# Optimization experiments

Hardware: AMD Instinct MI355X
Metric: run time of the kernel (lower is better)

Reference implementation:

```python
import jax, jax.numpy as jnp
import numpy as np

K = 7          # kernel_size
PAD = K // 2
NAZ, NEL = 12, 5
HID = 64
IC = 2         # input_channels == num_instruments
OC = 2         # output_channels (stereo)
EPS = 1e-5


def conv1d_same(x, w, b):
    # x: (N, Cin, T), w: (Cout, Cin, K) -> (N, Cout, T); cross-correlation like torch
    y = jax.lax.conv_general_dilated(x, w, (1,), 'SAME',
                                     dimension_numbers=('NCH', 'OIH', 'NCH'))
    return y + b[None, :, None]


def batchnorm(x, g, bt):
    # training-mode BatchNorm1d: biased batch stats over (N, T)
    mean = x.mean(axis=(0, 2), keepdims=True)
    var = x.var(axis=(0, 2), keepdims=True)
    return (x - mean) * jax.lax.rsqrt(var + EPS) * g[None, :, None] + bt[None, :, None]


def lrelu(x):
    return jnp.where(x >= 0, x, 0.2 * x)


def setup_inputs() -> dict:
    key = jax.random.key(0)
    ks = jax.random.split(key, 16)
    d = {}
    d['x'] = jax.random.normal(ks[0], (8, IC, 131072), dtype=jnp.float32)
    # spatial_param_net
    d['W1'] = jax.random.normal(ks[1], (HID, IC, K), dtype=jnp.float32) * 0.1
    d['b1'] = jnp.zeros((HID,), jnp.float32)
    d['g1'] = jnp.ones((HID,), jnp.float32)
    d['be1'] = jnp.zeros((HID,), jnp.float32)
    d['W2'] = jax.random.normal(ks[2], (2 * HID, HID, K), dtype=jnp.float32) * 0.05
    d['b2'] = jnp.zeros((2 * HID,), jnp.float32)
    d['g2'] = jnp.ones((2 * HID,), jnp.float32)
    d['be2'] = jnp.zeros((2 * HID,), jnp.float32)
    d['W3'] = jax.random.normal(ks[3], (IC * 3, 2 * HID, K), dtype=jnp.float32) * 0.05
    d['b3'] = jnp.zeros((IC * 3,), jnp.float32)
    # HRTF table: (num_azimuth*num_elevation, output_channels, K)
    d['hrtf'] = jax.random.normal(ks[4], (NAZ * NEL, OC, K), dtype=jnp.float32)
    # binaural_renderer (first conv in-channels = input_channels = 2)
    d['RW1'] = jax.random.normal(ks[5], (HID, IC, K), dtype=jnp.float32) * 0.1
    d['rb1'] = jnp.zeros((HID,), jnp.float32)
    d['rg1'] = jnp.ones((HID,), jnp.float32)
    d['rbe1'] = jnp.zeros((HID,), jnp.float32)
    d['RW2'] = jax.random.normal(ks[6], (2 * HID, HID, K), dtype=jnp.float32) * 0.05
    d['rb2'] = jnp.zeros((2 * HID,), jnp.float32)
    d['rg2'] = jnp.ones((2 * HID,), jnp.float32)
    d['rbe2'] = jnp.zeros((2 * HID,), jnp.float32)
    d['RW3'] = jax.random.normal(ks[7], (OC, 2 * HID, K), dtype=jnp.float32) * 0.05
    d['rb3'] = jnp.zeros((OC,), jnp.float32)
    return d


def reference(x, W1, b1, g1, be1, W2, b2, g2, be2, W3, b3, hrtf,
              RW1, rb1, rg1, rbe1, RW2, rb2, rg2, rbe2, RW3, rb3):
    B, I, T = x.shape
    # spatial parameter network
    h = lrelu(batchnorm(conv1d_same(x, W1, b1), g1, be1))
    h = lrelu(batchnorm(conv1d_same(h, W2, b2), g2, be2))
    sp = jnp.tanh(conv1d_same(h, W3, b3)).reshape(B, I, 3, T)
    # only t=0 of azimuth/elevation/distance is used (matches torch loop)
    az = (sp[:, :, 0, 0] + 1.0) * 0.5 * (NAZ - 1)
    el = (sp[:, :, 1, 0] + 1.0) * 0.5 * (NEL - 1)
    dist = (sp[:, :, 2, 0] + 1.0) * 0.5 * 0.9 + 0.1      # (B, I)
    az_i = jnp.clip(az.astype(jnp.int32), 0, NAZ - 1)
    el_i = jnp.clip(el.astype(jnp.int32), 0, NEL - 1)
    idx = el_i * NAZ + az_i                               # (B, I)
    wg = hrtf[idx]                                        # (B, I, OC, K) gathered filters
    # per-(b,i) conv1d with its gathered HRTF filter, scale by distance, sum over instruments
    xp = jnp.pad(x, ((0, 0), (0, 0), (PAD, PAD)))
    windows = jnp.stack([xp[:, :, k:k + T] for k in range(K)], axis=2)  # (B, I, K, T)
    summed = jnp.einsum('bikt,bick,bi->bct', windows, wg, dist)          # (B, OC, T)
    # binaural renderer
    h = lrelu(batchnorm(conv1d_same(summed, RW1, rb1), rg1, rbe1))
    h = lrelu(batchnorm(conv1d_same(h, RW2, rb2), rg2, rbe2))
    return jnp.tanh(conv1d_same(h, RW3, rb3))
```

## Files before the change

### kernel.cpp

```cpp
#include <hip/hip_runtime.h>
#include <hip/hip_fp16.h>
#include <cstddef>


#define TLEN 131072
#define NB 8
#define NICH 2
#define NHID 64
#define NH2 128
#define EPSV 1e-5f
#define CNTF 1048576.0f
#define FT 120
#define FGRID 1093
#define XCH 1024
#define NCH 128
#define XGRID 1024

typedef _Float16 f16x8 __attribute__((ext_vector_type(8)));
typedef float f32x4 __attribute__((ext_vector_type(4)));

__device__ __forceinline__ float lrelu(float v) { return fmaxf(v, 0.2f * v); }
__device__ __forceinline__ unsigned short h16(float v) {
  return __half_as_ushort(__float2half(v));
}
__device__ __forceinline__ float fh16(unsigned short u) {
  return __half2float(__ushort_as_half(u));
}
__device__ __forceinline__ float ftanh(float x) {
  float e = __expf(2.f * x);
  return 1.f - 2.f / (e + 1.f);
}

__global__ __launch_bounds__(256) void prep_weights(
    const float* __restrict__ W2c, const float* __restrict__ RW2c,
    const float* __restrict__ RW3c,
    const float* __restrict__ W1c, const float* __restrict__ RW1c,
    unsigned short* __restrict__ w2sp, unsigned short* __restrict__ w2re,
    unsigned short* __restrict__ w3g,
    unsigned short* __restrict__ w1sp, unsigned short* __restrict__ w1re)
{
  int e = blockIdx.x * 256 + threadIdx.x;
  if (e < 114688) {
    int e2 = (e >= 57344) ? e - 57344 : e;
    int frag = e2 >> 9, within = e2 & 511;
    int c = frag >> 3, mt = frag & 7;
    int mn = within >> 5, kk = within & 31;
    int o = mt * 16 + mn;
    int tap = c >> 1, ch = (c & 1) * 32 + kk;
    const float* src = (e >= 57344) ? RW2c : W2c;
    unsigned short* dst = (e >= 57344) ? w2re : w2sp;
    dst[e2] = h16(src[(o * 64 + ch) * 7 + tap]);
  } else if (e < 116736) {
    int e2 = e - 114688;
    int c = e2 >> 9, within = e2 & 511;
    int m = within >> 5, kk = within & 31;
    int ch = c * 32 + kk;
    w3g[e2] = (m < 14) ? h16(RW3c[((m / 7) * 128 + ch) * 7 + (m % 7)])
                       : (unsigned short)0;
  } else if (e < 120832) {
    int e2 = e - 116736;
    int which = (e2 >= 2048);
    int e3 = e2 & 2047;
    int m = e3 >> 9, w = e3 & 511;
    int mn = w >> 5, K = w & 31;
    int i = K >> 4, kk = K & 15;
    const float* src = which ? RW1c : W1c;
    unsigned short* dst = which ? w1re : w1sp;
    dst[e3] = (kk < 7) ? h16(src[(m * 16 + mn) * 14 + i * 7 + kk])
                       : (unsigned short)0;
  }
}

__global__ __launch_bounds__(256) void xcorr_stats(
    const float* __restrict__ z, float* __restrict__ partials)
{
  const int b = blockIdx.x >> 7;
  const int t0 = (blockIdx.x & (NCH - 1)) * XCH;
  __shared__ float zs[2][XCH + 8];
  __shared__ float redx[4][30];
  #pragma unroll
  for (int i = 0; i < 2; ++i) {
    const float* zp = &z[(size_t)(b * 2 + i) * TLEN + t0];
    *(float4*)&zs[i][threadIdx.x * 4] =
        *(const float4*)&zp[threadIdx.x * 4];
    if (threadIdx.x < 7) {
      int tg = t0 + XCH + threadIdx.x;
      zs[i][XCH + threadIdx.x] =
          (tg < TLEN) ? z[(size_t)(b * 2 + i) * TLEN + tg] : 0.f;
    }
    if (threadIdx.x == 7) zs[i][XCH + 7] = 0.f;
  }
  __syncthreads();

  float acc[30];
  #pragma unroll
  for (int q = 0; q < 30; ++q) acc[q] = 0.f;
  const int tb = threadIdx.x * 4;
  #pragma unroll
  for (int tt = 0; tt < 4; ++tt) {
    int j = tb + tt;
    float z0 = zs[0][j], z1 = zs[1][j];
    acc[28] += z0; acc[29] += z1;
    #pragma unroll
    for (int d = 0; d < 7; ++d) {
      float a0 = zs[0][j + d], a1 = zs[1][j + d];
      acc[d]      += z0 * a0;
      acc[7 + d]  += z0 * a1;
      acc[14 + d] += z1 * a0;
      acc[21 + d] += z1 * a1;
    }
  }
  #pragma unroll
  for (int q = 0; q < 30; ++q)
    #pragma unroll
    for (int m = 1; m <= 32; m <<= 1)
      acc[q] += __shfl_xor(acc[q], m, 64);
  const int lane = threadIdx.x & 63, wv = threadIdx.x >> 6;
  if (lane == 0)
    #pragma unroll
    for (int q = 0; q < 30; ++q) redx[wv][q] = acc[q];
  __syncthreads();
  if (threadIdx.x < 30)
    partials[blockIdx.x * 30 + threadIdx.x] =
        redx[0][threadIdx.x] + redx[1][threadIdx.x] +
        redx[2][threadIdx.x] + redx[3][threadIdx.x];
}

__global__ __launch_bounds__(256) void assemble_coef1(
    const float* __restrict__ partials, int nblocks,
    const float* __restrict__ W1c, const float* __restrict__ b1c,
    const float* __restrict__ g, const float* __restrict__ be,
    float* __restrict__ coef)
{
  __shared__ float R[30];
  __shared__ float pr[8][30];
  __shared__ float w1s[64 * 14];
  for (int e = threadIdx.x; e < 64 * 14; e += 256) w1s[e] = W1c[e];
  if (threadIdx.x < 240) {
    int q = threadIdx.x % 30, chunk = threadIdx.x / 30;
    float s = 0.f;
    for (int j = chunk; j < nblocks; j += 8) s += partials[j * 30 + q];
    pr[chunk][q] = s;
  }
  __syncthreads();
  if (threadIdx.x < 30) {
    float s = 0.f;
    #pragma unroll
    for (int c = 0; c < 8; ++c) s += pr[c][threadIdx.x];
    R[threadIdx.x] = s;
  }
  __syncthreads();
  if (threadIdx.x < 64) {
    int o = threadIdx.x;
    const float* w = &w1s[o * 14];
    float b1v = b1c[o];
    float sy = 0.f;
    #pragma unroll
    for (int i = 0; i < 2; ++i)
      #pragma unroll
      for (int k = 0; k < 7; ++k) sy += w[i * 7 + k] * R[28 + i];
    float syy = 0.f;
    #pragma unroll
    for (int i = 0; i < 2; ++i)
      #pragma unroll
      for (int k = 0; k < 7; ++k) {
        float wv = w[i * 7 + k];
        #pragma unroll
        for (int i2 = 0; i2 < 2; ++i2)
          #pragma unroll
          for (int k2 = 0; k2 < 7; ++k2) {
            int d = k2 - k;
            float r = (d >= 0) ? R[i * 14 + i2 * 7 + d]
                               : R[i2 * 14 + i * 7 - d];
            syy += wv * w[i2 * 7 + k2] * r;
          }
      }
    float S1 = CNTF * b1v + sy;
    float S2 = 2.f * b1v * S1 - CNTF * b1v * b1v + syy;
    float mean = S1 / CNTF;
    float var = S2 / CNTF - mean * mean;
    float a = g[o] * rsqrtf(var + EPSV);
    coef[o] = a;
    coef[64 + o] = be[o] - mean * a;
  }
}

__global__ __launch_bounds__(256) void reduce_coef(
    const float* __restrict__ partials, int nblocks, int C,
    const float* __restrict__ bso,
    const float* __restrict__ g, const float* __restrict__ be,
    float* __restrict__ coef)
{
  const int c = blockIdx.x;
  float s = 0.f, ss = 0.f;
  for (int j = threadIdx.x; j < nblocks; j += 256) {
    s  += partials[j * 2 * C + c];
    ss += partials[j * 2 * C + C + c];
  }
  #pragma unroll
  for (int off = 32; off >= 1; off >>= 1) {
    s  += __shfl_down(s, off, 64);
    ss += __shfl_down(ss, off, 64);
  }
  __shared__ float rs[4], rss[4];
  const int lane = threadIdx.x & 63, wv = threadIdx.x >> 6;
  if (lane == 0) { rs[wv] = s; rss[wv] = ss; }
  __syncthreads();
  if (threadIdx.x == 0) {
    float st  = rs[0] + rs[1] + rs[2] + rs[3];
    float sst = rss[0] + rss[1] + rss[2] + rss[3];
    float mean = st / CNTF;
    float var  = sst / CNTF - mean * mean;
    float a = g[c] * rsqrtf(var + EPSV);
    float d = be[c] - mean * a;
    coef[c] = a;
    coef[C + c] = d;
    coef[2 * C + c] = d + a * bso[c];
  }
}

__device__ __forceinline__ void stage_x(
    int t0, int xoff, const float* __restrict__ xin, int b, float* xs)
{
  for (int e = threadIdx.x; e < 2 * 168; e += 256) {
    int i = e / 168, j = e % 168;
    int tg = t0 - xoff + j;
    xs[e] = (tg >= 0 && tg < TLEN) ? xin[(b * NICH + i) * TLEN + tg] : 0.f;
  }
}

template<int HOF>
__device__ __forceinline__ void h1_mfma(
    int t0, const float* xs, unsigned short* xw,
    const unsigned short* __restrict__ w1f,
    const float* __restrict__ coef1, const float* __restrict__ b1c,
    unsigned short* h1f)
{
  for (int e = threadIdx.x; e < 144 * 2; e += 256) {
    int n = e >> 1, i = e & 1;
    const float* xp = &xs[i * 168 + n];
    unsigned short hv[7];
    #pragma unroll
    for (int kk = 0; kk < 7; ++kk) hv[kk] = h16(xp[kk]);
    *(uint4*)(xw + n * 32 + i * 16) = make_uint4(
        hv[0] | ((unsigned)hv[1] << 16), hv[2] | ((unsigned)hv[3] << 16),
        hv[4] | ((unsigned)hv[5] << 16), (unsigned)hv[6]);
    *(uint4*)(xw + n * 32 + i * 16 + 8) = make_uint4(0, 0, 0, 0);
  }
  __syncthreads();

  const int lane = threadIdx.x & 63;
  const int wv = threadIdx.x >> 6;
  const int mn = lane & 15, quad = lane >> 4;
  f16x8 A1 = *(const f16x8*)(w1f + wv * 512 + mn * 32 + quad * 8);
  f32x4 acc1[9];
  #pragma unroll
  for (int nt = 0; nt < 9; ++nt) {
    f32x4 z = {0.f, 0.f, 0.f, 0.f};
    acc1[nt] = z;
  }
  #pragma unroll
  for (int nt = 0; nt < 9; ++nt) {
    f16x8 bb = *(const f16x8*)(xw + (nt * 16 + mn) * 32 + quad * 8);
    acc1[nt] = __builtin_amdgcn_mfma_f32_16x16x32_f16(A1, bb, acc1[nt], 0, 0, 0);
  }
  const int ch0 = wv * 16 + quad * 4;
  float a1v[4], dd[4];
  #pragma unroll
  for (int r = 0; r < 4; ++r) {
    a1v[r] = coef1[ch0 + r];
    dd[r]  = coef1[64 + ch0 + r] + a1v[r] * b1c[ch0 + r];
  }
  #pragma unroll
  for (int nt = 0; nt < 9; ++nt) {
    int n = nt * 16 + mn;
    int t = t0 - HOF + n;
    bool ok = (t >= 0) && (t < TLEN);
    unsigned us[4];
    #pragma unroll
    for (int r = 0; r < 4; ++r) {
      float v = lrelu(a1v[r] * acc1[nt][r] + dd[r]);
      us[r] = h16(ok ? v : 0.f);
    }
    *(uint2*)(h1f + n * 72 + ch0) =
        make_uint2(us[0] | (us[1] << 16), us[2] | (us[3] << 16));
  }
}

template<int SAVE>
__global__ __launch_bounds__(256, 4) void conv2_stats_mfma(
    const float* __restrict__ xin,
    const unsigned short* __restrict__ w1f, const float* __restrict__ b1c,
    const float* __restrict__ coef1,
    const unsigned short* __restrict__ w2f,
    const float* __restrict__ b2c,
    float* __restrict__ partials,
    unsigned short* __restrict__ h1out)
{
  const int b  = blockIdx.x >> 10;
  const int t0 = (blockIdx.x & 1023) * 128;

  __shared__ __align__(16) char smem[31296];
  unsigned short* h1f = (unsigned short*)smem;
  float* xs = (float*)(smem + 20736);
  unsigned short* xw = (unsigned short*)(smem + 22080);
  float* redS = (float*)smem;
  float* redSS= (float*)(smem + 8704);

  stage_x(t0, 6, xin, b, xs);
  __syncthreads();
  h1_mfma<3>(t0, xs, xw, w1f, coef1, b1c, h1f);
  __syncthreads();

  if (SAVE == 1) {
    for (int e = threadIdx.x; e < 1024; e += 256) {
      int row = e >> 3, c8 = (e & 7) * 8;
      *(uint4*)(h1out + ((size_t)(b * TLEN + t0 + row) * 64 + c8)) =
          *(const uint4*)(h1f + (row + 3) * 72 + c8);
    }
  }

  const int lane = threadIdx.x & 63;
  const int wv = threadIdx.x >> 6;
  const int mn = lane & 15, quad = lane >> 4;

  f32x4 acc[2][8];
  #pragma unroll
  for (int mt = 0; mt < 2; ++mt)
    #pragma unroll
    for (int nt = 0; nt < 8; ++nt) {
      f32x4 z = {0.f, 0.f, 0.f, 0.f};
      acc[mt][nt] = z;
    }

  f16x8 ca[2], na[2];
  auto loadA = [&](int c, f16x8 (&A)[2]) {
    #pragma unroll
    for (int mt = 0; mt < 2; ++mt)
      A[mt] = *(const f16x8*)(w2f + (c * 8 + wv * 2 + mt) * 512 + mn * 32 + quad * 8);
  };
  loadA(0, ca);
  #pragma unroll
  for (int c = 0; c < 14; ++c) {
    if (c < 13) loadA(c + 1, na);
    const int tap = c >> 1;
    const int ch0 = (c & 1) * 32 + quad * 8;
    #pragma unroll
    for (int nt = 0; nt < 8; ++nt) {
      f16x8 bb = *(const f16x8*)(h1f + (nt * 16 + mn + tap) * 72 + ch0);
      acc[0][nt] = __builtin_amdgcn_mfma_f32_16x16x32_f16(ca[0], bb, acc[0][nt], 0, 0, 0);
      acc[1][nt] = __builtin_amdgcn_mfma_f32_16x16x32_f16(ca[1], bb, acc[1][nt], 0, 0, 0);
    }
    ca[0] = na[0]; ca[1] = na[1];
  }
  __syncthreads();

  #pragma unroll
  for (int mt = 0; mt < 2; ++mt)
    #pragma unroll
    for (int r = 0; r < 4; ++r) {
      int o = (wv * 2 + mt) * 16 + quad * 4 + r;
      float bo = b2c[o];
      float s = 0.f, ss = 0.f;
      #pragma unroll
      for (int nt = 0; nt < 8; ++nt) {
        float v = acc[mt][nt][r] + bo;
        s += v; ss += v * v;
      }
      redS[o * 17 + mn] = s;
      redSS[o * 17 + mn] = ss;
    }
  __syncthreads();
  {
    int o = threadIdx.x & 127;
    const float* src = (threadIdx.x < 128) ? redS : redSS;
    float s = 0.f;
    #pragma unroll
    for (int j = 0; j < 16; ++j) s += src[o * 17 + j];
    partials[blockIdx.x * 256 + threadIdx.x] = s;
  }
}

__global__ __launch_bounds__(256) void finalize_spatial(
    const float* __restrict__ x,
    const float* __restrict__ W1c, const float* __restrict__ b1c,
    const float* __restrict__ coef1,
    const float* __restrict__ W2c, const float* __restrict__ b2c,
    const float* __restrict__ coef2,
    const float* __restrict__ W3c, const float* __restrict__ b3c,
    const float* __restrict__ hrtf, float* __restrict__ wgbuf)
{
  const int bb = blockIdx.x;
  __shared__ float xl[2 * 16];
  __shared__ float h1l[64 * 10];
  __shared__ float h2l[NH2 * 4];
  __shared__ float sp[6];
  const int tid = threadIdx.x;
  if (tid < 32) {
    int i = tid >> 4, j = tid & 15;
    int t = j - 6;
    xl[tid] = (t >= 0) ? x[(bb * 2 + i) * TLEN + t] : 0.f;
  }
  __syncthreads();
  if (tid < 64) {
    int ch = tid;
    float a1 = coef1[ch], d1 = coef1[64 + ch], bo = b1c[ch];
    for (int tt = 0; tt < 10; ++tt) {
      float acc = bo;
      #pragma unroll
      for (int i2 = 0; i2 < 2; ++i2)
        #pragma unroll
        for (int k = 0; k < 7; ++k)
          acc += xl[i2 * 16 + tt + k] * W1c[ch * 14 + i2 * 7 + k];
      float v = lrelu(a1 * acc + d1);
      h1l[ch * 10 + tt] = (tt >= 3) ? v : 0.f;
    }
  }
  __syncthreads();
  if (tid < NH2) {
    int o = tid;
    float a2 = coef2[o], d2 = coef2[NH2 + o], bo = b2c[o];
    float acc[4] = {bo, bo, bo, bo};
    for (int i = 0; i < 64; ++i)
      #pragma unroll
      for (int k = 0; k < 7; ++k) {
        float w = W2c[(o * 64 + i) * 7 + k];
        #pragma unroll
        for (int t = 0; t < 4; ++t)
          acc[t] += h1l[i * 10 + t + k] * w;
      }
    #pragma unroll
    for (int t = 0; t < 4; ++t)
      h2l[o * 4 + t] = lrelu(a2 * acc[t] + d2);
  }
  __syncthreads();
  if (tid < 6) {
    int c3 = tid;
    float acc = b3c[c3];
    for (int c = 0; c < NH2; ++c)
      #pragma unroll
      for (int k = 3; k < 7; ++k)
        acc += h2l[c * 4 + (k - 3)] * W3c[(c3 * NH2 + c) * 7 + k];
    sp[c3] = tanhf(acc);
  }
  __syncthreads();
  if (tid < 2) {
    int i = tid;
    float az = (sp[i * 3 + 0] + 1.f) * 0.5f * 11.f;
    float el = (sp[i * 3 + 1] + 1.f) * 0.5f * 4.f;
    float dist = (sp[i * 3 + 2] + 1.f) * 0.5f * 0.9f + 0.1f;
    int azi = min(max((int)az, 0), 11);
    int eli = min(max((int)el, 0), 4);
    int idx = eli * 12 + azi;
    for (int e = 0; e < 14; ++e)
      wgbuf[(bb * 2 + i) * 14 + e] = hrtf[idx * 14 + e] * dist;
  }
}

__global__ __launch_bounds__(256) void mix_xcorr(
    const float* __restrict__ x, const float* __restrict__ wgbuf,
    float* __restrict__ summed, float* __restrict__ partials)
{
  const int b = blockIdx.x >> 7;
  const int t0 = (blockIdx.x & (NCH - 1)) * XCH;
  const int tid = threadIdx.x;
  __shared__ float xs2[2][XCH + 20];
  __shared__ float zs[2][XCH + 8];
  __shared__ float redx[4][30];

  float wv[2][2][7];
  #pragma unroll
  for (int i = 0; i < 2; ++i)
    #pragma unroll
    for (int c = 0; c < 2; ++c)
      #pragma unroll
      for (int k = 0; k < 7; ++k)
        wv[i][c][k] = wgbuf[(b * 2 + i) * 14 + c * 7 + k];

  const bool interior = (t0 >= 8) && (t0 + XCH + 12 <= TLEN);
  if (interior) {
    #pragma unroll
    for (int i = 0; i < 2; ++i) {
      const float* xp = &x[(size_t)(b * 2 + i) * TLEN + t0 - 8];
      *(float4*)&xs2[i][tid * 4] = *(const float4*)&xp[tid * 4];
      if (tid < 5)
        *(float4*)&xs2[i][XCH + tid * 4] = *(const float4*)&xp[XCH + tid * 4];
    }
  } else {
    for (int e = tid; e < 2 * (XCH + 20); e += 256) {
      int i = e / (XCH + 20), j = e % (XCH + 20);
      int tg = t0 - 8 + j;
      xs2[i][j] = (tg >= 0 && tg < TLEN) ? x[(size_t)(b * 2 + i) * TLEN + tg]
                                         : 0.f;
    }
  }
  __syncthreads();

  const int tb = tid * 4;
  {
    float xl[2][10];
    #pragma unroll
    for (int i = 0; i < 2; ++i)
      #pragma unroll
      for (int j = 0; j < 10; ++j) xl[i][j] = xs2[i][tb + 5 + j];
    float acc[2][4] = {{0.f, 0.f, 0.f, 0.f}, {0.f, 0.f, 0.f, 0.f}};
    #pragma unroll
    for (int i = 0; i < 2; ++i)
      #pragma unroll
      for (int c = 0; c < 2; ++c)
        #pragma unroll
        for (int k = 0; k < 7; ++k)
          #pragma unroll
          for (int tt = 0; tt < 4; ++tt)
            acc[c][tt] += xl[i][tt + k] * wv[i][c][k];
    #pragma unroll
    for (int c = 0; c < 2; ++c) {
      *(float4*)&zs[c][tb] =
          make_float4(acc[c][0], acc[c][1], acc[c][2], acc[c][3]);
      *reinterpret_cast<float4*>(&summed[(size_t)(b * 2 + c) * TLEN + t0 + tb]) =
          make_float4(acc[c][0], acc[c][1], acc[c][2], acc[c][3]);
    }
  }
  if (tid < 7) {
    int t = t0 + XCH + tid;
    float s0 = 0.f, s1 = 0.f;
    if (t < TLEN) {
      #pragma unroll
      for (int i = 0; i < 2; ++i)
        #pragma unroll
        for (int k = 0; k < 7; ++k) {
          float xv = xs2[i][XCH + tid + 5 + k];
          s0 += xv * wv[i][0][k];
          s1 += xv * wv[i][1][k];
        }
    }
    zs[0][XCH + tid] = s0;
    zs[1][XCH + tid] = s1;
  }
  if (tid == 7) { zs[0][XCH + 7] = 0.f; zs[1][XCH + 7] = 0.f; }
  __syncthreads();

  float acc[30];
  #pragma unroll
  for (int q = 0; q < 30; ++q) acc[q] = 0.f;
  #pragma unroll
  for (int tt = 0; tt < 4; ++tt) {
    int j = tb + tt;
    float z0 = zs[0][j], z1 = zs[1][j];
    acc[28] += z0; acc[29] += z1;
    #pragma unroll
    for (int d = 0; d < 7; ++d) {
      float a0 = zs[0][j + d], a1 = zs[1][j + d];
      acc[d]      += z0 * a0;
      acc[7 + d]  += z0 * a1;
      acc[14 + d] += z1 * a0;
      acc[21 + d] += z1 * a1;
    }
  }
  #pragma unroll
  for (int q = 0; q < 30; ++q)
    #pragma unroll
    for (int m = 1; m <= 32; m <<= 1)
      acc[q] += __shfl_xor(acc[q], m, 64);
  const int lane = tid & 63, wvx = tid >> 6;
  if (lane == 0)
    #pragma unroll
    for (int q = 0; q < 30; ++q) redx[wvx][q] = acc[q];
  __syncthreads();
  if (tid < 30)
    partials[blockIdx.x * 30 + tid] =
        redx[0][tid] + redx[1][tid] + redx[2][tid] + redx[3][tid];
}

__device__ __forceinline__ void final_tail(
    int b, int t0, f32x4 (&acc)[2][8],
    const float* __restrict__ coef2,
    const unsigned short* __restrict__ w3g, const float* __restrict__ rb3c,
    unsigned short* h2t, unsigned short* dq, float* __restrict__ out)
{
  const int lane = threadIdx.x & 63;
  const int wv = threadIdx.x >> 6;
  const int mn = lane & 15, quad = lane >> 4;

  float a2v[2][4], dd2[2][4];
  #pragma unroll
  for (int mt = 0; mt < 2; ++mt)
    #pragma unroll
    for (int r = 0; r < 4; ++r) {
      int o = (wv * 2 + mt) * 16 + quad * 4 + r;
      a2v[mt][r] = coef2[o];
      dd2[mt][r] = coef2[2 * NH2 + o];
    }
  __syncthreads();

  #pragma unroll
  for (int nt = 0; nt < 8; ++nt) {
    int jp = nt * 16 + mn;
    int t = t0 - 3 + jp;
    bool ok = (t >= 0) && (t < TLEN);
    #pragma unroll
    for (int mt = 0; mt < 2; ++mt) {
      int obase = (wv * 2 + mt) * 16 + quad * 4;
      unsigned us[4];
      #pragma unroll
      for (int r = 0; r < 4; ++r) {
        float v = lrelu(a2v[mt][r] * acc[mt][nt][r] + dd2[mt][r]);
        us[r] = h16(ok ? v : 0.f);
      }
      *(uint2*)(h2t + jp * 136 + obase) =
          make_uint2(us[0] | (us[1] << 16), us[2] | (us[3] << 16));
    }
  }
  __syncthreads();

  const int nt0 = wv * 2;
  f32x4 acc3[2];
  #pragma unroll
  for (int i = 0; i < 2; ++i) {
    f32x4 z = {0.f, 0.f, 0.f, 0.f};
    acc3[i] = z;
  }
  #pragma unroll
  for (int c = 0; c < 4; ++c) {
    f16x8 A3 = *(const f16x8*)(w3g + c * 512 + mn * 32 + quad * 8);
    #pragma unroll
    for (int i = 0; i < 2; ++i) {
      f16x8 bb = *(const f16x8*)(h2t + ((nt0 + i) * 16 + mn) * 136 + c * 32 + quad * 8);
      acc3[i] = __builtin_amdgcn_mfma_f32_16x16x32_f16(A3, bb, acc3[i], 0, 0, 0);
    }
  }
  #pragma unroll
  for (int i = 0; i < 2; ++i) {
    int n = (nt0 + i) * 16 + mn;
    unsigned us[4];
    #pragma unroll
    for (int r = 0; r < 4; ++r) us[r] = h16(acc3[i][r]);
    *(uint2*)(dq + n * 20 + quad * 4) =
        make_uint2(us[0] | (us[1] << 16), us[2] | (us[3] << 16));
  }
  __syncthreads();

  {
    int tid = threadIdx.x;
    if (tid < 240) {
      int oc = (tid >= FT) ? 1 : 0;
      int u = tid - oc * FT;
      float s = rb3c[oc];
      #pragma unroll
      for (int tap = 0; tap < 7; ++tap)
        s += fh16(dq[(u + tap) * 20 + oc * 7 + tap]);
      int t = t0 + u;
      if (t < TLEN) out[(b * 2 + oc) * TLEN + t] = ftanh(s);
    }
  }
}

__device__ __forceinline__ void conv2_loop(
    const unsigned short* h1f, const unsigned short* __restrict__ w2f,
    f32x4 (&acc)[2][8])
{
  const int lane = threadIdx.x & 63;
  const int wv = threadIdx.x >> 6;
  const int mn = lane & 15, quad = lane >> 4;
  #pragma unroll
  for (int mt = 0; mt < 2; ++mt)
    #pragma unroll
    for (int nt = 0; nt < 8; ++nt) {
      f32x4 z = {0.f, 0.f, 0.f, 0.f};
      acc[mt][nt] = z;
    }
  f16x8 ca[2], na[2];
  auto loadA = [&](int c, f16x8 (&A)[2]) {
    #pragma unroll
    for (int mt = 0; mt < 2; ++mt)
      A[mt] = *(const f16x8*)(w2f + (c * 8 + wv * 2 + mt) * 512 + mn * 32 + quad * 8);
  };
  loadA(0, ca);
  #pragma unroll
  for (int c = 0; c < 14; ++c) {
    if (c < 13) loadA(c + 1, na);
    const int tap = c >> 1;
    const int ch0 = (c & 1) * 32 + quad * 8;
    #pragma unroll
    for (int nt = 0; nt < 8; ++nt) {
      f16x8 bb = *(const f16x8*)(h1f + (nt * 16 + mn + tap) * 72 + ch0);
      acc[0][nt] = __builtin_amdgcn_mfma_f32_16x16x32_f16(ca[0], bb, acc[0][nt], 0, 0, 0);
      acc[1][nt] = __builtin_amdgcn_mfma_f32_16x16x32_f16(ca[1], bb, acc[1][nt], 0, 0, 0);
    }
    ca[0] = na[0]; ca[1] = na[1];
  }
}

__global__ __launch_bounds__(256, 4) void conv2_final_mfma(
    const float* __restrict__ xin,
    const unsigned short* __restrict__ w1f, const float* __restrict__ b1c,
    const float* __restrict__ coef1,
    const unsigned short* __restrict__ w2f,
    const float* __restrict__ coef2,
    const unsigned short* __restrict__ w3g, const float* __restrict__ rb3c,
    float* __restrict__ out)
{
  const int b  = blockIdx.y;
  const int t0 = blockIdx.x * FT;

  __shared__ __align__(16) char smem[39936];
  unsigned short* h1f = (unsigned short*)smem;
  float* xs = (float*)(smem + 20736);
  unsigned short* xw = (unsigned short*)(smem + 22080);
  unsigned short* h2t = (unsigned short*)smem;
  unsigned short* dq  = (unsigned short*)(smem + 34816);

  stage_x(t0, 9, xin, b, xs);
  __syncthreads();
  h1_mfma<6>(t0, xs, xw, w1f, coef1, b1c, h1f);
  __syncthreads();

  f32x4 acc[2][8];
  conv2_loop(h1f, w2f, acc);
  final_tail(b, t0, acc, coef2, w3g, rb3c, h2t, dq, out);
}

__global__ __launch_bounds__(256, 4) void conv2_final_h1(
    const unsigned short* __restrict__ h1g,
    const unsigned short* __restrict__ w2f,
    const float* __restrict__ coef2,
    const unsigned short* __restrict__ w3g, const float* __restrict__ rb3c,
    float* __restrict__ out)
{
  const int b  = blockIdx.y;
  const int t0 = blockIdx.x * FT;

  __shared__ __align__(16) char smem[39936];
  unsigned short* h1f = (unsigned short*)smem;
  unsigned short* h2t = (unsigned short*)smem;
  unsigned short* dq  = (unsigned short*)(smem + 34816);

  for (int e = threadIdx.x; e < 144 * 8; e += 256) {
    int r = e >> 3, c8 = (e & 7) * 8;
    int t = t0 - 6 + r;
    uint4 v = make_uint4(0, 0, 0, 0);
    if (t >= 0 && t < TLEN)
      v = *(const uint4*)(h1g + ((size_t)(b * TLEN + t) * 64 + c8));
    *(uint4*)(h1f + r * 72 + c8) = v;
  }
  __syncthreads();

  f32x4 acc[2][8];
  conv2_loop(h1f, w2f, acc);
  final_tail(b, t0, acc, coef2, w3g, rb3c, h2t, dq, out);
}

extern "C" void kernel_launch(void* const* d_in, const int* in_sizes, int n_in,
                              void* d_out, int out_size, void* d_ws, size_t ws_size,
                              hipStream_t stream)
{
  (void)in_sizes; (void)n_in; (void)out_size;
  const float* x    = (const float*)d_in[0];
  const float* W1   = (const float*)d_in[1];
  const float* b1   = (const float*)d_in[2];
  const float* g1   = (const float*)d_in[3];
  const float* be1  = (const float*)d_in[4];
  const float* W2   = (const float*)d_in[5];
  const float* b2   = (const float*)d_in[6];
  const float* g2   = (const float*)d_in[7];
  const float* be2  = (const float*)d_in[8];
  const float* W3   = (const float*)d_in[9];
  const float* b3   = (const float*)d_in[10];
  const float* hrtf = (const float*)d_in[11];
  const float* RW1  = (const float*)d_in[12];
  const float* rb1  = (const float*)d_in[13];
  const float* rg1  = (const float*)d_in[14];
  const float* rbe1 = (const float*)d_in[15];
  const float* RW2  = (const float*)d_in[16];
  const float* rb2  = (const float*)d_in[17];
  const float* rg2  = (const float*)d_in[18];
  const float* rbe2 = (const float*)d_in[19];
  const float* RW3  = (const float*)d_in[20];
  const float* rb3  = (const float*)d_in[21];
  float* out = (float*)d_out;

  float* partialsB = (float*)d_out;

  char* ws = (char*)d_ws;
  float* partialsA      = (float*)(ws + 0);
  float* summed         = (float*)(ws + 524288);
  float* coef1          = (float*)(ws + 8912896);
  float* coef2          = (float*)(ws + 8913408);
  float* coefR1         = (float*)(ws + 8914944);
  float* coefR2         = (float*)(ws + 8915456);
  float* wgbuf          = (float*)(ws + 8916992);
  unsigned short* w2sp  = (unsigned short*)(ws + 8918016);
  unsigned short* w2re  = (unsigned short*)(ws + 9032704);
  unsigned short* w3g   = (unsigned short*)(ws + 9147392);
  unsigned short* w1sp  = (unsigned short*)(ws + 9151488);
  unsigned short* w1re  = (unsigned short*)(ws + 9155584);
  unsigned short* h1g   = (unsigned short*)(ws + 16777216);
  const size_t WS_NEEDED_MID = 16777216ull + 134217728ull;
  const bool mid = ws_size >= WS_NEEDED_MID;

  prep_weights<<<472, 256, 0, stream>>>(W2, RW2, RW3, W1, RW1,
                                        w2sp, w2re, w3g, w1sp, w1re);
  xcorr_stats<<<XGRID, 256, 0, stream>>>(x, partialsA);
  assemble_coef1<<<1, 256, 0, stream>>>(partialsA, XGRID, W1, b1, g1, be1, coef1);
  conv2_stats_mfma<0><<<8192, 256, 0, stream>>>(x, w1sp, b1, coef1, w2sp,
                                                b2, partialsB, nullptr);
  reduce_coef<<<128, 256, 0, stream>>>(partialsB, 8192, 128, b2, g2, be2, coef2);
  finalize_spatial<<<8, 256, 0, stream>>>(x, W1, b1, coef1, W2, b2, coef2,
                                          W3, b3, hrtf, wgbuf);
  mix_xcorr<<<XGRID, 256, 0, stream>>>(x, wgbuf, summed, partialsA);
  assemble_coef1<<<1, 256, 0, stream>>>(partialsA, XGRID, RW1, rb1, rg1, rbe1, coefR1);
  if (mid) {
    conv2_stats_mfma<1><<<8192, 256, 0, stream>>>(summed, w1re, rb1, coefR1,
                                                  w2re, rb2, partialsB, h1g);
  } else {
    conv2_stats_mfma<0><<<8192, 256, 0, stream>>>(summed, w1re, rb1, coefR1,
                                                  w2re, rb2, partialsB, nullptr);
  }
  reduce_coef<<<128, 256, 0, stream>>>(partialsB, 8192, 128, rb2, rg2, rbe2, coefR2);
  if (mid) {
    conv2_final_h1<<<dim3(FGRID, NB), 256, 0, stream>>>(
        h1g, w2re, coefR2, w3g, rb3, out);
  } else {
    conv2_final_mfma<<<dim3(FGRID, NB), 256, 0, stream>>>(
        summed, w1re, rb1, coefR1, w2re, coefR2, w3g, rb3, out);
  }
}
```

Baseline: 617.0 us.

## Fuse weight prep into xcorr kernel and parallelize partial-sum reduction

Merges the weight-conversion kernel into the cross-correlation stats kernel as extra blocks, removing one launch. The single-block partial reduction inside assemble_coef1 becomes a separate 30-block reduce30 kernel, so the 1024x30 partials are summed in parallel. The in-block shuffle reduction is shortened to 16-lane groups with a 16-row shared-memory final sum. This trades one serialized single-block loop for an extra launch.

```diff
diff --git a/kernel.cpp b/kernel.cpp
--- a/kernel.cpp
+++ b/kernel.cpp
@@ -15,6 +15,7 @@
 #define XCH 1024
 #define NCH 128
 #define XGRID 1024
+#define PREPB 472
 
 typedef _Float16 f16x8 __attribute__((ext_vector_type(8)));
 typedef float f32x4 __attribute__((ext_vector_type(4)));
@@ -31,7 +32,8 @@
   return 1.f - 2.f / (e + 1.f);
 }
 
-__global__ __launch_bounds__(256) void prep_weights(
+__device__ __forceinline__ void prep_body(
+    int e,
     const float* __restrict__ W2c, const float* __restrict__ RW2c,
     const float* __restrict__ RW3c,
     const float* __restrict__ W1c, const float* __restrict__ RW1c,
@@ -39,7 +41,6 @@
     unsigned short* __restrict__ w3g,
     unsigned short* __restrict__ w1sp, unsigned short* __restrict__ w1re)
 {
-  int e = blockIdx.x * 256 + threadIdx.x;
   if (e < 114688) {
     int e2 = (e >= 57344) ? e - 57344 : e;
     int frag = e2 >> 9, within = e2 & 511;
@@ -71,18 +72,51 @@
   }
 }
 
-__global__ __launch_bounds__(256) void xcorr_stats(
-    const float* __restrict__ z, float* __restrict__ partials)
-{
+__device__ __forceinline__ void xcorr_reduce_tail(
+    float (&acc)[30], float (*redx)[30], float* __restrict__ partials)
+{
+  #pragma unroll
+  for (int q = 0; q < 30; ++q)
+    #pragma unroll
+    for (int m = 1; m <= 8; m <<= 1)
+      acc[q] += __shfl_xor(acc[q], m, 64);
+  const int lane = threadIdx.x & 63, wv = threadIdx.x >> 6;
+  if ((lane & 15) == 0) {
+    int row = wv * 4 + (lane >> 4);
+    #pragma unroll
+    for (int q = 0; q < 30; ++q) redx[row][q] = acc[q];
+  }
+  __syncthreads();
+  if (threadIdx.x < 30) {
+    float s = 0.f;
+    #pragma unroll
+    for (int r = 0; r < 16; ++r) s += redx[r][threadIdx.x];
+    partials[blockIdx.x * 30 + threadIdx.x] = s;
+  }
+}
+
+__global__ __launch_bounds__(256) void xcorr_prep(
+    const float* __restrict__ z, float* __restrict__ partials,
+    const float* __restrict__ W2c, const float* __restrict__ RW2c,
+    const float* __restrict__ RW3c,
+    const float* __restrict__ W1c, const float* __restrict__ RW1c,
+    unsigned short* __restrict__ w2sp, unsigned short* __restrict__ w2re,
+    unsigned short* __restrict__ w3g,
+    unsigned short* __restrict__ w1sp, unsigned short* __restrict__ w1re)
+{
+  if (blockIdx.x >= XGRID) {
+    int e = (blockIdx.x - XGRID) * 256 + threadIdx.x;
+    prep_body(e, W2c, RW2c, RW3c, W1c, RW1c, w2sp, w2re, w3g, w1sp, w1re);
+    return;
+  }
   const int b = blockIdx.x >> 7;
   const int t0 = (blockIdx.x & (NCH - 1)) * XCH;
   __shared__ float zs[2][XCH + 8];
-  __shared__ float redx[4][30];
+  __shared__ float redx[16][30];
   #pragma unroll
   for (int i = 0; i < 2; ++i) {
     const float* zp = &z[(size_t)(b * 2 + i) * TLEN + t0];
-    *(float4*)&zs[i][threadIdx.x * 4] =
-        *(const float4*)&zp[threadIdx.x * 4];
+    *(float4*)&zs[i][threadIdx.x * 4] = *(const float4*)&zp[threadIdx.x * 4];
     if (threadIdx.x < 7) {
       int tg = t0 + XCH + threadIdx.x;
       zs[i][XCH + threadIdx.x] =
@@ -110,45 +144,34 @@
       acc[21 + d] += z1 * a1;
     }
   }
-  #pragma unroll
-  for (int q = 0; q < 30; ++q)
-    #pragma unroll
-    for (int m = 1; m <= 32; m <<= 1)
-      acc[q] += __shfl_xor(acc[q], m, 64);
-  const int lane = threadIdx.x & 63, wv = threadIdx.x >> 6;
-  if (lane == 0)
-    #pragma unroll
-    for (int q = 0; q < 30; ++q) redx[wv][q] = acc[q];
-  __syncthreads();
-  if (threadIdx.x < 30)
-    partials[blockIdx.x * 30 + threadIdx.x] =
-        redx[0][threadIdx.x] + redx[1][threadIdx.x] +
-        redx[2][threadIdx.x] + redx[3][threadIdx.x];
+  xcorr_reduce_tail(acc, redx, partials);
+}
+
+__global__ __launch_bounds__(256) void reduce30(
+    const float* __restrict__ partials, int nblocks, float* __restrict__ R)
+{
+  const int q = blockIdx.x;
+  float s = 0.f;
+  for (int j = threadIdx.x; j < nblocks; j += 256)
+    s += partials[j * 30 + q];
+  #pragma unroll
+  for (int m = 1; m <= 32; m <<= 1) s += __shfl_xor(s, m, 64);
+  __shared__ float rs[4];
+  if ((threadIdx.x & 63) == 0) rs[threadIdx.x >> 6] = s;
+  __syncthreads();
+  if (threadIdx.x == 0) R[q] = rs[0] + rs[1] + rs[2] + rs[3];
 }
 
 __global__ __launch_bounds__(256) void assemble_coef1(
-    const float* __restrict__ partials, int nblocks,
+    const float* __restrict__ Rg,
     const float* __restrict__ W1c, const float* __restrict__ b1c,
     const float* __restrict__ g, const float* __restrict__ be,
     float* __restrict__ coef)
 {
   __shared__ float R[30];
-  __shared__ float pr[8][30];
   __shared__ float w1s[64 * 14];
   for (int e = threadIdx.x; e < 64 * 14; e += 256) w1s[e] = W1c[e];
-  if (threadIdx.x < 240) {
-    int q = threadIdx.x % 30, chunk = threadIdx.x / 30;
-    float s = 0.f;
-    for (int j = chunk; j < nblocks; j += 8) s += partials[j * 30 + q];
-    pr[chunk][q] = s;
-  }
-  __syncthreads();
-  if (threadIdx.x < 30) {
-    float s = 0.f;
-    #pragma unroll
-    for (int c = 0; c < 8; ++c) s += pr[c][threadIdx.x];
-    R[threadIdx.x] = s;
-  }
+  if (threadIdx.x < 30) R[threadIdx.x] = Rg[threadIdx.x];
   __syncthreads();
   if (threadIdx.x < 64) {
     int o = threadIdx.x;
@@ -466,7 +489,7 @@
   const int tid = threadIdx.x;
   __shared__ float xs2[2][XCH + 20];
   __shared__ float zs[2][XCH + 8];
-  __shared__ float redx[4][30];
+  __shared__ float redx[16][30];
 
   float wv[2][2][7];
   #pragma unroll
@@ -557,19 +580,7 @@
       acc[21 + d] += z1 * a1;
     }
   }
-  #pragma unroll
-  for (int q = 0; q < 30; ++q)
-    #pragma unroll
-    for (int m = 1; m <= 32; m <<= 1)
-      acc[q] += __shfl_xor(acc[q], m, 64);
-  const int lane = tid & 63, wvx = tid >> 6;
-  if (lane == 0)
-    #pragma unroll
-    for (int q = 0; q < 30; ++q) redx[wvx][q] = acc[q];
-  __syncthreads();
-  if (tid < 30)
-    partials[blockIdx.x * 30 + tid] =
-        redx[0][tid] + redx[1][tid] + redx[2][tid] + redx[3][tid];
+  xcorr_reduce_tail(acc, redx, partials);
 }
 
 __device__ __forceinline__ void final_tail(
@@ -794,21 +805,23 @@
   unsigned short* w3g   = (unsigned short*)(ws + 9147392);
   unsigned short* w1sp  = (unsigned short*)(ws + 9151488);
   unsigned short* w1re  = (unsigned short*)(ws + 9155584);
+  float* Rbuf           = (float*)(ws + 9159680);
   unsigned short* h1g   = (unsigned short*)(ws + 16777216);
   const size_t WS_NEEDED_MID = 16777216ull + 134217728ull;
   const bool mid = ws_size >= WS_NEEDED_MID;
 
-  prep_weights<<<472, 256, 0, stream>>>(W2, RW2, RW3, W1, RW1,
-                                        w2sp, w2re, w3g, w1sp, w1re);
-  xcorr_stats<<<XGRID, 256, 0, stream>>>(x, partialsA);
-  assemble_coef1<<<1, 256, 0, stream>>>(partialsA, XGRID, W1, b1, g1, be1, coef1);
+  xcorr_prep<<<XGRID + PREPB, 256, 0, stream>>>(
+      x, partialsA, W2, RW2, RW3, W1, RW1, w2sp, w2re, w3g, w1sp, w1re);
+  reduce30<<<30, 256, 0, stream>>>(partialsA, XGRID, Rbuf);
+  assemble_coef1<<<1, 256, 0, stream>>>(Rbuf, W1, b1, g1, be1, coef1);
   conv2_stats_mfma<0><<<8192, 256, 0, stream>>>(x, w1sp, b1, coef1, w2sp,
                                                 b2, partialsB, nullptr);
   reduce_coef<<<128, 256, 0, stream>>>(partialsB, 8192, 128, b2, g2, be2, coef2);
   finalize_spatial<<<8, 256, 0, stream>>>(x, W1, b1, coef1, W2, b2, coef2,
                                           W3, b3, hrtf, wgbuf);
   mix_xcorr<<<XGRID, 256, 0, stream>>>(x, wgbuf, summed, partialsA);
-  assemble_coef1<<<1, 256, 0, stream>>>(partialsA, XGRID, RW1, rb1, rg1, rbe1, coefR1);
+  reduce30<<<30, 256, 0, stream>>>(partialsA, XGRID, Rbuf);
+  assemble_coef1<<<1, 256, 0, stream>>>(Rbuf, RW1, rb1, rg1, rbe1, coefR1);
   if (mid) {
     conv2_stats_mfma<1><<<8192, 256, 0, stream>>>(summed, w1re, rb1, coefR1,
                                                   w2re, rb2, partialsB, h1g);
```

After: 571.0 us, median of 2. -7.4%, faster.
